# Performance work log

Measured on AMD Instinct MI355X. Metric: run time of the kernel, lower is better.

## Reference

```python
import jax, jax.numpy as jnp
import numpy as np

N_NODES = 8192
HIDDEN = 256
HEADS = 4
HEAD_DIM = HIDDEN // HEADS
NUM_EDGES = 4096
NUM_INC = 65536
LN_EPS = 1e-5


def setup_inputs() -> dict:
    key = jax.random.key(0)
    ks = jax.random.split(key, 8)
    scale = HIDDEN ** -0.5
    return {
        "x": jax.random.normal(ks[0], (N_NODES, HIDDEN), jnp.float32),
        "node_idx": jax.random.randint(ks[1], (NUM_INC,), 0, N_NODES),
        "edge_idx": jax.random.randint(ks[2], (NUM_INC,), 0, NUM_EDGES),
        "W_w": jax.random.normal(ks[3], (HIDDEN, HIDDEN), jnp.float32) * scale,
        "W_b": jax.random.normal(ks[4], (HIDDEN,), jnp.float32) * 0.02,
        "edge_att": jax.random.normal(ks[5], (HEADS, HEAD_DIM), jnp.float32) * scale,
        "out_w": jax.random.normal(ks[6], (HIDDEN, HIDDEN), jnp.float32) * scale,
        "out_b": jax.random.normal(ks[7], (HIDDEN,), jnp.float32) * 0.02,
    }


def reference(x, node_idx, edge_idx, W_w, W_b, edge_att, out_w, out_b):
    n = x.shape[0]
    e = node_idx.shape[0]
    # x' = W(x), split into heads: [N, heads, head_dim]
    xw = (x @ W_w.T + W_b).reshape(n, HEADS, HEAD_DIM)
    feat = xw[node_idx]                                   # [E, heads, hd]
    logits = jnp.einsum("ehd,hd->eh", feat, edge_att)      # [E, heads]
    # segment softmax over nodes within each hyperedge, per head
    seg_max = jax.ops.segment_max(logits, edge_idx, num_segments=NUM_EDGES)
    p = jnp.exp(logits - seg_max[edge_idx])
    seg_sum = jax.ops.segment_sum(p, edge_idx, num_segments=NUM_EDGES)
    attn = p / seg_sum[edge_idx]                           # [E, heads]
    attn_mean = attn.mean(axis=1)                          # mean over heads, [E]
    # hyperedges with < 2 nodes are skipped in the original
    sizes = jax.ops.segment_sum(jnp.ones((e,), x.dtype), edge_idx, num_segments=NUM_EDGES)
    valid = sizes[edge_idx] >= 2.0
    attn_mean = jnp.where(valid, attn_mean, 0.0)
    # scatter-add attention-weighted ORIGINAL features back to nodes
    contrib = attn_mean[:, None] * x[node_idx]             # [E, H]
    out = jnp.zeros_like(x).at[node_idx].add(contrib)
    # degree normalization counts ALL incidences (including size-1 edges)
    counts = jnp.zeros((n,), x.dtype).at[node_idx].add(1.0)
    out = out / jnp.clip(counts, 1.0)[:, None]
    out = out @ out_w.T + out_b
    # fresh nn.LayerNorm => affine identity, biased variance, eps=1e-5
    mu = out.mean(-1, keepdims=True)
    var = ((out - mu) ** 2).mean(-1, keepdims=True)
    out = (out - mu) / jnp.sqrt(var + LN_EPS)
    # NxN pairwise attention accumulation: AW[i,j] = sum_e attn_i(e)*count_j(e), diag zeroed
    A = jnp.zeros((n, NUM_EDGES), x.dtype).at[node_idx, edge_idx].add(attn_mean)
    B = jnp.zeros((n, NUM_EDGES), x.dtype).at[node_idx, edge_idx].add(1.0)
    attention_weights = A @ B.T
    attention_weights = attention_weights.at[jnp.diag_indices(n)].set(0.0)
    return out, attention_weights
```

## Files before the change

### kernel.cpp

```cpp
#include <hip/hip_runtime.h>
#include <stdint.h>

#define N_NODES  8192
#define HIDDEN   256
#define HEADS    4
#define HEAD_DIM 64
#define NUM_EDGES 4096
#define NUM_INC  65536
#define LN_EPS   1e-5f

typedef unsigned int uint_t;
typedef float __attribute__((ext_vector_type(4))) f4v;


#define OFF_SEGSZ    0
#define OFF_NCNT     16384
#define OFF_NFILL    49152
#define OFF_EFILL    81920
#define OFF_SEGSUM   98304
#define ZERO_BYTES   163840
#define OFF_VKH      163840
#define OFF_BL       167936
#define OFF_LOGIT    168192
#define OFF_NPTR     299264
#define OFF_EPTR     332288
#define OFF_NINC     348928
#define OFF_EMEM     611072

__global__ __launch_bounds__(256) void k_foldzero(const float* __restrict__ Ww,
                                                  const float* __restrict__ Wb,
                                                  const float* __restrict__ ea,
                                                  float* __restrict__ vkhT,
                                                  float* __restrict__ bl,
                                                  uint_t* __restrict__ zw) {
    int t = threadIdx.x, b = blockIdx.x;
    zw[b * 256 + t] = 0u;
    if (b < HEADS) {
        int k = t, h = b;
        float a = 0.f;
        for (int d = 0; d < HEAD_DIM; ++d)
            a += ea[h * HEAD_DIM + d] * Ww[(size_t)(h * HEAD_DIM + d) * HIDDEN + k];
        vkhT[h * HIDDEN + k] = a;
        if (k == 0) {
            float s = 0.f;
            for (int d = 0; d < HEAD_DIM; ++d)
                s += Wb[h * HEAD_DIM + d] * ea[h * HEAD_DIM + d];
            bl[h] = s;
        }
    }
}

__global__ __launch_bounds__(256) void k_logits(const float* __restrict__ x,
                                                const float* __restrict__ vkhT,
                                                const float* __restrict__ bl,
                                                const int* __restrict__ node_idx,
                                                const int* __restrict__ edge_idx,
                                                int* __restrict__ seg_size,
                                                int* __restrict__ node_cnt,
                                                float* __restrict__ logit) {
    __shared__ __align__(16) float xs[32 * HIDDEN];
    __shared__ __align__(16) float vs[HEADS * HIDDEN];
    __shared__ float bls[HEADS];
    int t = threadIdx.x, b = blockIdx.x;
    {
        int i = b * 256 + t;
        atomicAdd(&seg_size[edge_idx[i]], 1);
        atomicAdd(&node_cnt[node_idx[i]], 1);
    }
    float4* xsv = (float4*)xs;
    const float4* xg = (const float4*)(x + (size_t)b * 32 * HIDDEN);
    #pragma unroll
    for (int i = 0; i < 8; ++i) xsv[i * 256 + t] = xg[i * 256 + t];
    ((float4*)vs)[t] = ((const float4*)vkhT)[t];
    if (t < HEADS) bls[t] = bl[t];
    __syncthreads();
    if (t < 128) {
        int n = t >> 2, h = t & 3;
        const float4* xr = (const float4*)(xs + n * HIDDEN);
        const float4* vr = (const float4*)(vs + h * HIDDEN);
        float acc = bls[h];
        for (int k4 = 0; k4 < HIDDEN / 4; ++k4) {
            float4 xv = xr[k4], vv = vr[k4];
            acc += xv.x * vv.x + xv.y * vv.y + xv.z * vv.z + xv.w * vv.w;
        }
        logit[(b * 32 + n) * HEADS + h] = acc;
    }
}

__global__ __launch_bounds__(256) void k_scan(const int* __restrict__ node_cnt, int* __restrict__ node_ptr,
                                              const int* __restrict__ seg_size, int* __restrict__ edge_ptr) {
    __shared__ int part[256];
    const int* cnt; int* ptr; int n;
    if (blockIdx.x == 0) { cnt = node_cnt; ptr = node_ptr; n = N_NODES; }
    else                 { cnt = seg_size; ptr = edge_ptr; n = NUM_EDGES; }
    int t = threadIdx.x, C = n / 256;
    int s = 0;
    for (int j = 0; j < C; ++j) s += cnt[t * C + j];
    part[t] = s;
    __syncthreads();
    if (t == 0) {
        int run = 0;
        for (int i = 0; i < 256; ++i) { int tmp = part[i]; part[i] = run; run += tmp; }
        ptr[n] = run;
    }
    __syncthreads();
    int run = part[t];
    for (int j = 0; j < C; ++j) { ptr[t * C + j] = run; run += cnt[t * C + j]; }
}

__global__ void k_fill(const int* __restrict__ node_idx, const int* __restrict__ edge_idx,
                       const int* __restrict__ node_ptr, const int* __restrict__ edge_ptr,
                       int* __restrict__ node_fill, int* __restrict__ edge_fill,
                       int* __restrict__ node_inc, int* __restrict__ edge_mem,
                       const float* __restrict__ logit, float* __restrict__ seg_sum) {
    int i = blockIdx.x * 256 + threadIdx.x;
    int n = node_idx[i], e = edge_idx[i];
    int p = node_ptr[n] + atomicAdd(&node_fill[n], 1);
    node_inc[p] = i;
    int q = edge_ptr[e] + atomicAdd(&edge_fill[e], 1);
    edge_mem[q] = n;
    const float4 lg = *(const float4*)(logit + (size_t)n * 4);
    atomicAdd(&seg_sum[e * 4 + 0], __expf(lg.x));
    atomicAdd(&seg_sum[e * 4 + 1], __expf(lg.y));
    atomicAdd(&seg_sum[e * 4 + 2], __expf(lg.z));
    atomicAdd(&seg_sum[e * 4 + 3], __expf(lg.w));
}

__global__ __launch_bounds__(256) void k_aw_out(const int* __restrict__ node_ptr,
                                                const int* __restrict__ node_inc,
                                                const int* __restrict__ edge_idx,
                                                const int* __restrict__ edge_ptr,
                                                const int* __restrict__ edge_mem,
                                                const float* __restrict__ logit,
                                                const float* __restrict__ seg_sum,
                                                const float* __restrict__ x,
                                                const float* __restrict__ out_w,
                                                const float* __restrict__ out_b,
                                                float* __restrict__ AW,
                                                float* __restrict__ out0) {
    __shared__ __align__(16) float buf[N_NODES];
    __shared__ float sr[16], mu_s[16], rs_s[16];
    int t = threadIdx.x, w = t >> 6, lane = t & 63;
    int b = blockIdx.x;

    if (b >= 512) {
        int i = b - 512;
        int pb = node_ptr[i], pe = node_ptr[i + 1];
        const float4 lg = *(const float4*)(logit + (size_t)i * 4);
        float ex0 = __expf(lg.x), ex1 = __expf(lg.y);
        float ex2 = __expf(lg.z), ex3 = __expf(lg.w);
        float4* rowv = (float4*)buf;
        #pragma unroll
        for (int c = 0; c < 8; ++c) rowv[c * 256 + t] = make_float4(0.f, 0.f, 0.f, 0.f);
        int p = pb + w;
        int m_nxt = (p < pe) ? node_inc[p] : 0;
        __syncthreads();
        for (; p < pe; p += 4) {
            int m = m_nxt;
            if (p + 4 < pe) m_nxt = node_inc[p + 4];
            int e = edge_idx[m];
            int qb = edge_ptr[e], qe = edge_ptr[e + 1];
            if (qe - qb >= 2) {
                const float4 ss = *(const float4*)(seg_sum + (size_t)e * 4);
                float a = 0.25f * (ex0 / ss.x + ex1 / ss.y + ex2 / ss.z + ex3 / ss.w);
                for (int q = qb + lane; q < qe; q += 64)
                    atomicAdd(&buf[edge_mem[q]], a);
            }
        }
        __syncthreads();
        if (t == 0) buf[i] = 0.f;
        __syncthreads();
        f4v* dst = (f4v*)(AW + (size_t)i * N_NODES);
        #pragma unroll
        for (int c = 0; c < 8; ++c)
            __builtin_nontemporal_store(((const f4v*)rowv)[c * 256 + t], &dst[c * 256 + t]);
        return;
    }

    float (*y)[260] = (float (*)[260])buf;
    int R = b * 16;
    {
        int nl = t >> 4, s = t & 15;
        int n = R + nl;
        int nb = node_ptr[n], ne = node_ptr[n + 1];
        const float4 lg = *(const float4*)(logit + (size_t)n * 4);
        float ex0 = __expf(lg.x), ex1 = __expf(lg.y);
        float ex2 = __expf(lg.z), ex3 = __expf(lg.w);
        float wsum = 0.f;
        for (int p = nb + s; p < ne; p += 16) {
            int m = node_inc[p];
            int e = edge_idx[m];
            int qb = edge_ptr[e], qe = edge_ptr[e + 1];
            if (qe - qb >= 2) {
                const float4 ss = *(const float4*)(seg_sum + (size_t)e * 4);
                wsum += 0.25f * (ex0 / ss.x + ex1 / ss.y + ex2 / ss.z + ex3 / ss.w);
            }
        }
        #pragma unroll
        for (int off = 1; off < 16; off <<= 1) wsum += __shfl_xor(wsum, off, 64);
        if (s == 0) {
            int c = ne - nb; if (c < 1) c = 1;
            sr[nl] = wsum / (float)c;
        }
    }
    __syncthreads();
    #pragma unroll
    for (int r = 0; r < 16; ++r)
        y[r][t] = sr[r] * x[(size_t)(R + r) * HIDDEN + t];
    __syncthreads();
    float acc[16];
    float bias = out_b[t];
    #pragma unroll
    for (int r = 0; r < 16; ++r) acc[r] = bias;
    const float4* wr4 = (const float4*)(out_w + (size_t)t * HIDDEN);
    for (int j4 = 0; j4 < HIDDEN / 4; ++j4) {
        float4 wv = wr4[j4];
        #pragma unroll
        for (int r = 0; r < 16; ++r) {
            float4 yv = *(const float4*)&y[r][j4 * 4];
            acc[r] += yv.x * wv.x + yv.y * wv.y + yv.z * wv.z + yv.w * wv.w;
        }
    }
    __syncthreads();
    #pragma unroll
    for (int r = 0; r < 16; ++r) y[r][t] = acc[r];
    __syncthreads();
    #pragma unroll
    for (int rr = 0; rr < 4; ++rr) {
        int r = (w << 2) | rr;
        float v = y[r][lane] + y[r][lane + 64] + y[r][lane + 128] + y[r][lane + 192];
        #pragma unroll
        for (int off = 32; off; off >>= 1) v += __shfl_down(v, off, 64);
        float mu = __shfl(v, 0, 64) * (1.0f / HIDDEN);
        float d0 = y[r][lane] - mu, d1 = y[r][lane + 64] - mu;
        float d2 = y[r][lane + 128] - mu, d3 = y[r][lane + 192] - mu;
        float s2 = d0 * d0 + d1 * d1 + d2 * d2 + d3 * d3;
        #pragma unroll
        for (int off = 32; off; off >>= 1) s2 += __shfl_down(s2, off, 64);
        if (lane == 0) {
            mu_s[r] = mu;
            rs_s[r] = rsqrtf(s2 * (1.0f / HIDDEN) + LN_EPS);
        }
    }
    __syncthreads();
    #pragma unroll
    for (int r = 0; r < 16; ++r)
        out0[(size_t)(R + r) * HIDDEN + t] = (y[r][t] - mu_s[r]) * rs_s[r];
}

extern "C" void kernel_launch(void* const* d_in, const int* in_sizes, int n_in,
                              void* d_out, int out_size, void* d_ws, size_t ws_size,
                              hipStream_t stream) {
    const float* x        = (const float*)d_in[0];
    const int*   node_idx = (const int*)d_in[1];
    const int*   edge_idx = (const int*)d_in[2];
    const float* Ww       = (const float*)d_in[3];
    const float* Wb       = (const float*)d_in[4];
    const float* ea       = (const float*)d_in[5];
    const float* ow       = (const float*)d_in[6];
    const float* ob       = (const float*)d_in[7];
    float* out0 = (float*)d_out;
    float* aw   = out0 + (size_t)N_NODES * HIDDEN;

    char* ws = (char*)d_ws;
    int*    seg_size  = (int*)(ws + OFF_SEGSZ);
    int*    node_cnt  = (int*)(ws + OFF_NCNT);
    int*    node_fill = (int*)(ws + OFF_NFILL);
    int*    edge_fill = (int*)(ws + OFF_EFILL);
    float*  seg_sum   = (float*)(ws + OFF_SEGSUM);
    float*  vkhT      = (float*)(ws + OFF_VKH);
    float*  bl        = (float*)(ws + OFF_BL);
    float*  logit     = (float*)(ws + OFF_LOGIT);
    int*    node_ptr  = (int*)(ws + OFF_NPTR);
    int*    edge_ptr  = (int*)(ws + OFF_EPTR);
    int*    node_inc  = (int*)(ws + OFF_NINC);
    int*    edge_mem  = (int*)(ws + OFF_EMEM);

    k_foldzero<<<ZERO_BYTES / 4 / 256, 256, 0, stream>>>(Ww, Wb, ea, vkhT, bl, (uint_t*)ws);
    k_logits<<<N_NODES / 32, 256, 0, stream>>>(x, vkhT, bl, node_idx, edge_idx,
                                               seg_size, node_cnt, logit);
    k_scan<<<2, 256, 0, stream>>>(node_cnt, node_ptr, seg_size, edge_ptr);
    k_fill<<<NUM_INC / 256, 256, 0, stream>>>(node_idx, edge_idx, node_ptr, edge_ptr,
                                              node_fill, edge_fill, node_inc, edge_mem,
                                              logit, seg_sum);
    k_aw_out<<<N_NODES + 512, 256, 0, stream>>>(node_ptr, node_inc, edge_idx, edge_ptr,
                                                edge_mem, logit, seg_sum, x, ow, ob, aw, out0);
}
```

Baseline: 368.3 us.

## Fuse all stages into one cooperative persistent kernel with work queue

Merges the five separate kernels (zero/fold, logits, scan, fill, AW/output) into a single cooperative kernel that separates the stages with grid-wide syncs. The final stage becomes a persistent loop in which blocks pull work items from an atomic counter. The grid is sized from the occupancy query, capped at 4 blocks per CU across 256 CUs. This is meant to remove kernel launch gaps and balance the irregular per-node AW work. In exchange it adds grid-barrier cost, an atomic fetch per work item, and lower per-block occupancy limits.

Result: slower. 641.4 us (+74.1%).

```diff
diff --git a/kernel.cpp b/kernel.cpp
--- a/kernel.cpp
+++ b/kernel.cpp
@@ -1,5 +1,8 @@
 #include <hip/hip_runtime.h>
+#include <hip/hip_cooperative_groups.h>
 #include <stdint.h>
+
+namespace cg = cooperative_groups;
 
 #define N_NODES  8192
 #define HIDDEN   256
@@ -18,23 +21,50 @@
 #define OFF_NFILL    49152
 #define OFF_EFILL    81920
 #define OFF_SEGSUM   98304
-#define ZERO_BYTES   163840
-#define OFF_VKH      163840
-#define OFF_BL       167936
-#define OFF_LOGIT    168192
-#define OFF_NPTR     299264
-#define OFF_EPTR     332288
-#define OFF_NINC     348928
-#define OFF_EMEM     611072
-
-__global__ __launch_bounds__(256) void k_foldzero(const float* __restrict__ Ww,
-                                                  const float* __restrict__ Wb,
-                                                  const float* __restrict__ ea,
-                                                  float* __restrict__ vkhT,
-                                                  float* __restrict__ bl,
-                                                  uint_t* __restrict__ zw) {
+#define OFF_CTR      163840
+#define ZERO_BYTES   163856
+#define OFF_VKH      163856
+#define OFF_BL       167952
+#define OFF_LOGIT    168016
+#define OFF_NPTR     299088
+#define OFF_EPTR     331904
+#define OFF_NINC     348352
+#define OFF_EMEM     610496
+
+#define N_WORK (N_NODES + 512)
+
+__global__ __launch_bounds__(256, 4) void k_all(
+    const float* __restrict__ Ww, const float* __restrict__ Wb,
+    const float* __restrict__ ea, const float* __restrict__ x,
+    const int* __restrict__ node_idx, const int* __restrict__ edge_idx,
+    const float* __restrict__ out_w, const float* __restrict__ out_b,
+    char* __restrict__ ws, float* __restrict__ AW, float* __restrict__ out0)
+{
+    float* vkhT    = (float*)(ws + OFF_VKH);
+    float* bl      = (float*)(ws + OFF_BL);
+    float* logit   = (float*)(ws + OFF_LOGIT);
+    int*   seg_size  = (int*)(ws + OFF_SEGSZ);
+    int*   node_cnt  = (int*)(ws + OFF_NCNT);
+    int*   node_fill = (int*)(ws + OFF_NFILL);
+    int*   edge_fill = (int*)(ws + OFF_EFILL);
+    float* seg_sum   = (float*)(ws + OFF_SEGSUM);
+    int*   node_ptr  = (int*)(ws + OFF_NPTR);
+    int*   edge_ptr  = (int*)(ws + OFF_EPTR);
+    int*   node_inc  = (int*)(ws + OFF_NINC);
+    int*   edge_mem  = (int*)(ws + OFF_EMEM);
+    int*   wctr      = (int*)(ws + OFF_CTR);
+
+    __shared__ __align__(16) float smem[9232];
+    __shared__ float sr[16], mu_s[16], rs_s[16];
+    __shared__ int wks;
+
+    cg::grid_group gg = cg::this_grid();
     int t = threadIdx.x, b = blockIdx.x;
-    zw[b * 256 + t] = 0u;
+    int nb = gridDim.x;
+    int w = t >> 6, lane = t & 63;
+
+    for (int g = b * 256 + t; g < ZERO_BYTES / 4; g += nb * 256)
+        ((uint_t*)ws)[g] = 0u;
     if (b < HEADS) {
         int k = t, h = b;
         float a = 0.f;
@@ -48,204 +78,184 @@
             bl[h] = s;
         }
     }
-}
-
-__global__ __launch_bounds__(256) void k_logits(const float* __restrict__ x,
-                                                const float* __restrict__ vkhT,
-                                                const float* __restrict__ bl,
-                                                const int* __restrict__ node_idx,
-                                                const int* __restrict__ edge_idx,
-                                                int* __restrict__ seg_size,
-                                                int* __restrict__ node_cnt,
-                                                float* __restrict__ logit) {
-    __shared__ __align__(16) float xs[32 * HIDDEN];
-    __shared__ __align__(16) float vs[HEADS * HIDDEN];
-    __shared__ float bls[HEADS];
-    int t = threadIdx.x, b = blockIdx.x;
-    {
+    gg.sync();
+
+    if (b < 256) {
         int i = b * 256 + t;
         atomicAdd(&seg_size[edge_idx[i]], 1);
         atomicAdd(&node_cnt[node_idx[i]], 1);
-    }
-    float4* xsv = (float4*)xs;
-    const float4* xg = (const float4*)(x + (size_t)b * 32 * HIDDEN);
-    #pragma unroll
-    for (int i = 0; i < 8; ++i) xsv[i * 256 + t] = xg[i * 256 + t];
-    ((float4*)vs)[t] = ((const float4*)vkhT)[t];
-    if (t < HEADS) bls[t] = bl[t];
-    __syncthreads();
-    if (t < 128) {
-        int n = t >> 2, h = t & 3;
-        const float4* xr = (const float4*)(xs + n * HIDDEN);
-        const float4* vr = (const float4*)(vs + h * HIDDEN);
-        float acc = bls[h];
-        for (int k4 = 0; k4 < HIDDEN / 4; ++k4) {
-            float4 xv = xr[k4], vv = vr[k4];
-            acc += xv.x * vv.x + xv.y * vv.y + xv.z * vv.z + xv.w * vv.w;
-        }
-        logit[(b * 32 + n) * HEADS + h] = acc;
-    }
-}
-
-__global__ __launch_bounds__(256) void k_scan(const int* __restrict__ node_cnt, int* __restrict__ node_ptr,
-                                              const int* __restrict__ seg_size, int* __restrict__ edge_ptr) {
-    __shared__ int part[256];
-    const int* cnt; int* ptr; int n;
-    if (blockIdx.x == 0) { cnt = node_cnt; ptr = node_ptr; n = N_NODES; }
-    else                 { cnt = seg_size; ptr = edge_ptr; n = NUM_EDGES; }
-    int t = threadIdx.x, C = n / 256;
-    int s = 0;
-    for (int j = 0; j < C; ++j) s += cnt[t * C + j];
-    part[t] = s;
-    __syncthreads();
-    if (t == 0) {
-        int run = 0;
-        for (int i = 0; i < 256; ++i) { int tmp = part[i]; part[i] = run; run += tmp; }
-        ptr[n] = run;
-    }
-    __syncthreads();
-    int run = part[t];
-    for (int j = 0; j < C; ++j) { ptr[t * C + j] = run; run += cnt[t * C + j]; }
-}
-
-__global__ void k_fill(const int* __restrict__ node_idx, const int* __restrict__ edge_idx,
-                       const int* __restrict__ node_ptr, const int* __restrict__ edge_ptr,
-                       int* __restrict__ node_fill, int* __restrict__ edge_fill,
-                       int* __restrict__ node_inc, int* __restrict__ edge_mem,
-                       const float* __restrict__ logit, float* __restrict__ seg_sum) {
-    int i = blockIdx.x * 256 + threadIdx.x;
-    int n = node_idx[i], e = edge_idx[i];
-    int p = node_ptr[n] + atomicAdd(&node_fill[n], 1);
-    node_inc[p] = i;
-    int q = edge_ptr[e] + atomicAdd(&edge_fill[e], 1);
-    edge_mem[q] = n;
-    const float4 lg = *(const float4*)(logit + (size_t)n * 4);
-    atomicAdd(&seg_sum[e * 4 + 0], __expf(lg.x));
-    atomicAdd(&seg_sum[e * 4 + 1], __expf(lg.y));
-    atomicAdd(&seg_sum[e * 4 + 2], __expf(lg.z));
-    atomicAdd(&seg_sum[e * 4 + 3], __expf(lg.w));
-}
-
-__global__ __launch_bounds__(256) void k_aw_out(const int* __restrict__ node_ptr,
-                                                const int* __restrict__ node_inc,
-                                                const int* __restrict__ edge_idx,
-                                                const int* __restrict__ edge_ptr,
-                                                const int* __restrict__ edge_mem,
-                                                const float* __restrict__ logit,
-                                                const float* __restrict__ seg_sum,
-                                                const float* __restrict__ x,
-                                                const float* __restrict__ out_w,
-                                                const float* __restrict__ out_b,
-                                                float* __restrict__ AW,
-                                                float* __restrict__ out0) {
-    __shared__ __align__(16) float buf[N_NODES];
-    __shared__ float sr[16], mu_s[16], rs_s[16];
-    int t = threadIdx.x, w = t >> 6, lane = t & 63;
-    int b = blockIdx.x;
-
-    if (b >= 512) {
-        int i = b - 512;
-        int pb = node_ptr[i], pe = node_ptr[i + 1];
-        const float4 lg = *(const float4*)(logit + (size_t)i * 4);
-        float ex0 = __expf(lg.x), ex1 = __expf(lg.y);
-        float ex2 = __expf(lg.z), ex3 = __expf(lg.w);
-        float4* rowv = (float4*)buf;
-        #pragma unroll
-        for (int c = 0; c < 8; ++c) rowv[c * 256 + t] = make_float4(0.f, 0.f, 0.f, 0.f);
-        int p = pb + w;
-        int m_nxt = (p < pe) ? node_inc[p] : 0;
-        __syncthreads();
-        for (; p < pe; p += 4) {
-            int m = m_nxt;
-            if (p + 4 < pe) m_nxt = node_inc[p + 4];
-            int e = edge_idx[m];
-            int qb = edge_ptr[e], qe = edge_ptr[e + 1];
-            if (qe - qb >= 2) {
-                const float4 ss = *(const float4*)(seg_sum + (size_t)e * 4);
-                float a = 0.25f * (ex0 / ss.x + ex1 / ss.y + ex2 / ss.z + ex3 / ss.w);
-                for (int q = qb + lane; q < qe; q += 64)
-                    atomicAdd(&buf[edge_mem[q]], a);
-            }
-        }
-        __syncthreads();
-        if (t == 0) buf[i] = 0.f;
-        __syncthreads();
-        f4v* dst = (f4v*)(AW + (size_t)i * N_NODES);
-        #pragma unroll
-        for (int c = 0; c < 8; ++c)
-            __builtin_nontemporal_store(((const f4v*)rowv)[c * 256 + t], &dst[c * 256 + t]);
-        return;
-    }
-
-    float (*y)[260] = (float (*)[260])buf;
-    int R = b * 16;
-    {
-        int nl = t >> 4, s = t & 15;
-        int n = R + nl;
-        int nb = node_ptr[n], ne = node_ptr[n + 1];
+        float* xs  = smem;
+        float* vs  = smem + 8192;
+        float* bls = smem + 9216;
+        float4* xsv = (float4*)xs;
+        const float4* xg = (const float4*)(x + (size_t)b * 32 * HIDDEN);
+        #pragma unroll
+        for (int c = 0; c < 8; ++c) xsv[c * 256 + t] = xg[c * 256 + t];
+        ((float4*)vs)[t] = ((const float4*)vkhT)[t];
+        if (t < HEADS) bls[t] = bl[t];
+        __syncthreads();
+        if (t < 128) {
+            int n = t >> 2, h = t & 3;
+            const float4* xr = (const float4*)(xs + n * HIDDEN);
+            const float4* vr = (const float4*)(vs + h * HIDDEN);
+            float acc = bls[h];
+            for (int k4 = 0; k4 < HIDDEN / 4; ++k4) {
+                float4 xv = xr[k4], vv = vr[k4];
+                acc += xv.x * vv.x + xv.y * vv.y + xv.z * vv.z + xv.w * vv.w;
+            }
+            logit[(b * 32 + n) * HEADS + h] = acc;
+        }
+    }
+    gg.sync();
+
+    if (b < 2) {
+        int* part = (int*)smem;
+        const int* cnt; int* ptr; int n;
+        if (b == 0) { cnt = node_cnt; ptr = node_ptr; n = N_NODES; }
+        else        { cnt = seg_size; ptr = edge_ptr; n = NUM_EDGES; }
+        int C = n / 256;
+        int s = 0;
+        for (int j = 0; j < C; ++j) s += cnt[t * C + j];
+        part[t] = s;
+        __syncthreads();
+        if (t == 0) {
+            int run = 0;
+            for (int i = 0; i < 256; ++i) { int tmp = part[i]; part[i] = run; run += tmp; }
+            ptr[n] = run;
+        }
+        __syncthreads();
+        int run = part[t];
+        for (int j = 0; j < C; ++j) { ptr[t * C + j] = run; run += cnt[t * C + j]; }
+    }
+    gg.sync();
+
+    if (b < 256) {
+        int i = b * 256 + t;
+        int n = node_idx[i], e = edge_idx[i];
+        int p = node_ptr[n] + atomicAdd(&node_fill[n], 1);
+        node_inc[p] = i;
+        int q = edge_ptr[e] + atomicAdd(&edge_fill[e], 1);
+        edge_mem[q] = n;
         const float4 lg = *(const float4*)(logit + (size_t)n * 4);
-        float ex0 = __expf(lg.x), ex1 = __expf(lg.y);
-        float ex2 = __expf(lg.z), ex3 = __expf(lg.w);
-        float wsum = 0.f;
-        for (int p = nb + s; p < ne; p += 16) {
-            int m = node_inc[p];
-            int e = edge_idx[m];
-            int qb = edge_ptr[e], qe = edge_ptr[e + 1];
-            if (qe - qb >= 2) {
-                const float4 ss = *(const float4*)(seg_sum + (size_t)e * 4);
-                wsum += 0.25f * (ex0 / ss.x + ex1 / ss.y + ex2 / ss.z + ex3 / ss.w);
-            }
-        }
-        #pragma unroll
-        for (int off = 1; off < 16; off <<= 1) wsum += __shfl_xor(wsum, off, 64);
-        if (s == 0) {
-            int c = ne - nb; if (c < 1) c = 1;
-            sr[nl] = wsum / (float)c;
-        }
-    }
-    __syncthreads();
-    #pragma unroll
-    for (int r = 0; r < 16; ++r)
-        y[r][t] = sr[r] * x[(size_t)(R + r) * HIDDEN + t];
-    __syncthreads();
-    float acc[16];
-    float bias = out_b[t];
-    #pragma unroll
-    for (int r = 0; r < 16; ++r) acc[r] = bias;
-    const float4* wr4 = (const float4*)(out_w + (size_t)t * HIDDEN);
-    for (int j4 = 0; j4 < HIDDEN / 4; ++j4) {
-        float4 wv = wr4[j4];
-        #pragma unroll
-        for (int r = 0; r < 16; ++r) {
-            float4 yv = *(const float4*)&y[r][j4 * 4];
-            acc[r] += yv.x * wv.x + yv.y * wv.y + yv.z * wv.z + yv.w * wv.w;
-        }
-    }
-    __syncthreads();
-    #pragma unroll
-    for (int r = 0; r < 16; ++r) y[r][t] = acc[r];
-    __syncthreads();
-    #pragma unroll
-    for (int rr = 0; rr < 4; ++rr) {
-        int r = (w << 2) | rr;
-        float v = y[r][lane] + y[r][lane + 64] + y[r][lane + 128] + y[r][lane + 192];
-        #pragma unroll
-        for (int off = 32; off; off >>= 1) v += __shfl_down(v, off, 64);
-        float mu = __shfl(v, 0, 64) * (1.0f / HIDDEN);
-        float d0 = y[r][lane] - mu, d1 = y[r][lane + 64] - mu;
-        float d2 = y[r][lane + 128] - mu, d3 = y[r][lane + 192] - mu;
-        float s2 = d0 * d0 + d1 * d1 + d2 * d2 + d3 * d3;
-        #pragma unroll
-        for (int off = 32; off; off >>= 1) s2 += __shfl_down(s2, off, 64);
-        if (lane == 0) {
-            mu_s[r] = mu;
-            rs_s[r] = rsqrtf(s2 * (1.0f / HIDDEN) + LN_EPS);
-        }
-    }
-    __syncthreads();
-    #pragma unroll
-    for (int r = 0; r < 16; ++r)
-        out0[(size_t)(R + r) * HIDDEN + t] = (y[r][t] - mu_s[r]) * rs_s[r];
+        atomicAdd(&seg_sum[e * 4 + 0], __expf(lg.x));
+        atomicAdd(&seg_sum[e * 4 + 1], __expf(lg.y));
+        atomicAdd(&seg_sum[e * 4 + 2], __expf(lg.z));
+        atomicAdd(&seg_sum[e * 4 + 3], __expf(lg.w));
+    }
+    gg.sync();
+
+    for (;;) {
+        __syncthreads();
+        if (t == 0) wks = atomicAdd(wctr, 1);
+        __syncthreads();
+        int wk = wks;
+        if (wk >= N_WORK) break;
+
+        if (wk >= 512) {
+            int i = wk - 512;
+            int pb = node_ptr[i], pe = node_ptr[i + 1];
+            const float4 lg = *(const float4*)(logit + (size_t)i * 4);
+            float ex0 = __expf(lg.x), ex1 = __expf(lg.y);
+            float ex2 = __expf(lg.z), ex3 = __expf(lg.w);
+            float* buf = smem;
+            float4* rowv = (float4*)buf;
+            #pragma unroll
+            for (int c = 0; c < 8; ++c) rowv[c * 256 + t] = make_float4(0.f, 0.f, 0.f, 0.f);
+            int p = pb + w;
+            int m_nxt = (p < pe) ? node_inc[p] : 0;
+            __syncthreads();
+            for (; p < pe; p += 4) {
+                int m = m_nxt;
+                if (p + 4 < pe) m_nxt = node_inc[p + 4];
+                int e = edge_idx[m];
+                int qb = edge_ptr[e], qe = edge_ptr[e + 1];
+                if (qe - qb >= 2) {
+                    const float4 ss = *(const float4*)(seg_sum + (size_t)e * 4);
+                    float a = 0.25f * (ex0 / ss.x + ex1 / ss.y + ex2 / ss.z + ex3 / ss.w);
+                    for (int q = qb + lane; q < qe; q += 64)
+                        atomicAdd(&buf[edge_mem[q]], a);
+                }
+            }
+            __syncthreads();
+            if (t == 0) buf[i] = 0.f;
+            __syncthreads();
+            f4v* dst = (f4v*)(AW + (size_t)i * N_NODES);
+            #pragma unroll
+            for (int c = 0; c < 8; ++c)
+                __builtin_nontemporal_store(((const f4v*)rowv)[c * 256 + t], &dst[c * 256 + t]);
+            continue;
+        }
+
+        float (*y)[260] = (float (*)[260])smem;
+        int R = wk * 16;
+        {
+            int nl = t >> 4, s = t & 15;
+            int n = R + nl;
+            int nbg = node_ptr[n], ne = node_ptr[n + 1];
+            const float4 lg = *(const float4*)(logit + (size_t)n * 4);
+            float ex0 = __expf(lg.x), ex1 = __expf(lg.y);
+            float ex2 = __expf(lg.z), ex3 = __expf(lg.w);
+            float wsum = 0.f;
+            for (int p = nbg + s; p < ne; p += 16) {
+                int m = node_inc[p];
+                int e = edge_idx[m];
+                int qb = edge_ptr[e], qe = edge_ptr[e + 1];
+                if (qe - qb >= 2) {
+                    const float4 ss = *(const float4*)(seg_sum + (size_t)e * 4);
+                    wsum += 0.25f * (ex0 / ss.x + ex1 / ss.y + ex2 / ss.z + ex3 / ss.w);
+                }
+            }
+            #pragma unroll
+            for (int off = 1; off < 16; off <<= 1) wsum += __shfl_xor(wsum, off, 64);
+            if (s == 0) {
+                int c = ne - nbg; if (c < 1) c = 1;
+                sr[nl] = wsum / (float)c;
+            }
+        }
+        __syncthreads();
+        #pragma unroll
+        for (int r = 0; r < 16; ++r)
+            y[r][t] = sr[r] * x[(size_t)(R + r) * HIDDEN + t];
+        __syncthreads();
+        float acc[16];
+        float bias = out_b[t];
+        #pragma unroll
+        for (int r = 0; r < 16; ++r) acc[r] = bias;
+        const float4* wr4 = (const float4*)(out_w + (size_t)t * HIDDEN);
+        for (int j4 = 0; j4 < HIDDEN / 4; ++j4) {
+            float4 wv = wr4[j4];
+            #pragma unroll
+            for (int r = 0; r < 16; ++r) {
+                float4 yv = *(const float4*)&y[r][j4 * 4];
+                acc[r] += yv.x * wv.x + yv.y * wv.y + yv.z * wv.z + yv.w * wv.w;
+            }
+        }
+        __syncthreads();
+        #pragma unroll
+        for (int r = 0; r < 16; ++r) y[r][t] = acc[r];
+        __syncthreads();
+        #pragma unroll
+        for (int rr = 0; rr < 4; ++rr) {
+            int r = (w << 2) | rr;
+            float v = y[r][lane] + y[r][lane + 64] + y[r][lane + 128] + y[r][lane + 192];
+            #pragma unroll
+            for (int off = 32; off; off >>= 1) v += __shfl_down(v, off, 64);
+            float mu = __shfl(v, 0, 64) * (1.0f / HIDDEN);
+            float d0 = y[r][lane] - mu, d1 = y[r][lane + 64] - mu;
+            float d2 = y[r][lane + 128] - mu, d3 = y[r][lane + 192] - mu;
+            float s2 = d0 * d0 + d1 * d1 + d2 * d2 + d3 * d3;
+            #pragma unroll
+            for (int off = 32; off; off >>= 1) s2 += __shfl_down(s2, off, 64);
+            if (lane == 0) {
+                mu_s[r] = mu;
+                rs_s[r] = rsqrtf(s2 * (1.0f / HIDDEN) + LN_EPS);
+            }
+        }
+        __syncthreads();
+        #pragma unroll
+        for (int r = 0; r < 16; ++r)
+            out0[(size_t)(R + r) * HIDDEN + t] = (y[r][t] - mu_s[r]) * rs_s[r];
+    }
 }
 
 extern "C" void kernel_launch(void* const* d_in, const int* in_sizes, int n_in,
@@ -261,28 +271,21 @@
     const float* ob       = (const float*)d_in[7];
     float* out0 = (float*)d_out;
     float* aw   = out0 + (size_t)N_NODES * HIDDEN;
-
-    char* ws = (char*)d_ws;
-    int*    seg_size  = (int*)(ws + OFF_SEGSZ);
-    int*    node_cnt  = (int*)(ws + OFF_NCNT);
-    int*    node_fill = (int*)(ws + OFF_NFILL);
-    int*    edge_fill = (int*)(ws + OFF_EFILL);
-    float*  seg_sum   = (float*)(ws + OFF_SEGSUM);
-    float*  vkhT      = (float*)(ws + OFF_VKH);
-    float*  bl        = (float*)(ws + OFF_BL);
-    float*  logit     = (float*)(ws + OFF_LOGIT);
-    int*    node_ptr  = (int*)(ws + OFF_NPTR);
-    int*    edge_ptr  = (int*)(ws + OFF_EPTR);
-    int*    node_inc  = (int*)(ws + OFF_NINC);
-    int*    edge_mem  = (int*)(ws + OFF_EMEM);
-
-    k_foldzero<<<ZERO_BYTES / 4 / 256, 256, 0, stream>>>(Ww, Wb, ea, vkhT, bl, (uint_t*)ws);
-    k_logits<<<N_NODES / 32, 256, 0, stream>>>(x, vkhT, bl, node_idx, edge_idx,
-                                               seg_size, node_cnt, logit);
-    k_scan<<<2, 256, 0, stream>>>(node_cnt, node_ptr, seg_size, edge_ptr);
-    k_fill<<<NUM_INC / 256, 256, 0, stream>>>(node_idx, edge_idx, node_ptr, edge_ptr,
-                                              node_fill, edge_fill, node_inc, edge_mem,
-                                              logit, seg_sum);
-    k_aw_out<<<N_NODES + 512, 256, 0, stream>>>(node_ptr, node_inc, edge_idx, edge_ptr,
-                                                edge_mem, logit, seg_sum, x, ow, ob, aw, out0);
+    char*  ws   = (char*)d_ws;
+
+    static int nblk = 0;
+    if (nblk == 0) {
+        int nper = 0;
+        hipOccupancyMaxActiveBlocksPerMultiprocessor(&nper, k_all, 256, 0);
+        if (nper < 1) nper = 1;
+        if (nper > 4) nper = 4;
+        nblk = nper * 256;
+    }
+
+    void* args[] = {
+        (void*)&Ww, (void*)&Wb, (void*)&ea, (void*)&x,
+        (void*)&node_idx, (void*)&edge_idx, (void*)&ow, (void*)&ob,
+        (void*)&ws, (void*)&aw, (void*)&out0
+    };
+    hipLaunchCooperativeKernel((void*)k_all, dim3(nblk), dim3(256), args, 0, stream);
 }
```
